# Kernel optimization log

Hardware: AMD Instinct MI355X
Metric: run time of the kernel (lower is better)

## Reference

```python
import jax, jax.numpy as jnp
import numpy as np
from jax import lax

B, DIN, DOUT, DEPTH = 4096, 2048, 2048, 16


def setup_inputs() -> dict:
    key = jax.random.key(0)
    k1, k2, k3, k4 = jax.random.split(key, 4)
    return {
        "x": jax.random.normal(k1, (B, DIN), jnp.float32),
        "absolute_weights": jax.random.normal(k2, (DEPTH, DIN, DOUT), jnp.float32),
        "classical_weights": jax.random.normal(k3, (DIN, DOUT), jnp.float32),
        "classical_biases": jax.random.normal(k4, (DOUT,), jnp.float32),
    }


def _absolute_probs(W):
    # W: [depth, din, dout]; the torch code indexes W[d, j, g] with j over
    # output dims and g in {0,1,2} (3 gates per depth step).
    din = W.shape[1]
    dout = DOUT
    # angles per output j, flattened over (depth, gate): [dout, depth*3]
    ang = jnp.transpose(W[:, :dout, :3], (1, 0, 2)).reshape(dout, -1)
    s0 = jnp.ones((din,), W.dtype) / np.float32(np.sqrt(din))

    def step(s, a):
        # The dense "rotation" matrix built in torch is: diag=cos,
        # superdiag (wrapped) = -sin, subdiag (wrapped) = +sin, i.e.
        # (M s)[i] = cos*s[i] - sin*s[(i+1)%n] + sin*s[(i-1)%n].
        c, si = jnp.cos(a), jnp.sin(a)
        s_new = c * s - si * jnp.roll(s, -1) + si * jnp.roll(s, 1)
        return s_new, None

    def per_j(angs):
        s, _ = lax.scan(step, s0, angs)
        return jnp.abs(s[0]) ** 2

    return jax.vmap(per_j)(ang)  # [dout]


def reference(x, absolute_weights, classical_weights, classical_biases):
    classical = x @ classical_weights + classical_biases  # [B, dout]
    probs = _absolute_probs(absolute_weights)             # [dout], batch-independent
    return jnp.tanh(classical + probs[None, :])
```

## Files before the change

kernel.cpp:

```cpp
#include <hip/hip_runtime.h>
#include <math.h>

#define BATCH 4096
#define DIN   2048
#define DOUT  2048
#define DEPTH 16

typedef unsigned short u16;
typedef __attribute__((ext_vector_type(8))) short short8;
typedef __attribute__((ext_vector_type(16))) float f32x16;


__device__ static inline unsigned bf16_rn(float x) {
    unsigned u = __float_as_uint(x);
    return (u + 0x7FFFu + ((u >> 16) & 1u)) >> 16;
}

__device__ static inline float tanh_fast(float z) {
    float zc = fminf(fmaxf(z, -15.0f), 15.0f);
    float e = __builtin_amdgcn_exp2f(zc * 2.8853900817779268f);
    return (e - 1.0f) * __builtin_amdgcn_rcpf(e + 1.0f);
}

__device__ static inline void async16(u16* lds, const u16* g) {
    __builtin_amdgcn_global_load_lds(
        (const __attribute__((address_space(1))) void*)g,
        (__attribute__((address_space(3))) void*)lds, 16, 0, 0);
}

__global__ __launch_bounds__(256) void probs_kernel(const float* __restrict__ W,
                                                    float* __restrict__ probs) {
    int tid = threadIdx.x;
    int jl = tid >> 4, d = tid & 15;
    int j = blockIdx.x * 16 + jl;
    const float* p = W + (size_t)d * DIN * DOUT + (size_t)j * DOUT;
    float pr = cosf(p[0]) * cosf(p[1]) * cosf(p[2]);
#pragma unroll
    for (int off = 1; off < 16; off <<= 1) pr *= __shfl_xor(pr, off, 16);
    if (d == 0) probs[j] = pr * pr * (1.0f / (float)DIN);
}

__global__ __launch_bounds__(256) void convert_x_kernel(const float* __restrict__ x,
                                                        u16* __restrict__ xh,
                                                        u16* __restrict__ xl) {
    int i = (blockIdx.x * 256 + threadIdx.x) * 4;
    float4 v = *(const float4*)(x + i);
    float vv[4] = {v.x, v.y, v.z, v.w};
    u16 hh[4], ll[4];
#pragma unroll
    for (int c = 0; c < 4; ++c) {
        unsigned hb = bf16_rn(vv[c]);
        hh[c] = (u16)hb;
        float r = vv[c] - __uint_as_float(hb << 16);
        ll[c] = (u16)bf16_rn(r);
    }
    ushort4 h, l;
    h.x = hh[0]; h.y = hh[1]; h.z = hh[2]; h.w = hh[3];
    l.x = ll[0]; l.y = ll[1]; l.z = ll[2]; l.w = ll[3];
    *(ushort4*)(xh + i) = h;
    *(ushort4*)(xl + i) = l;
}

__global__ __launch_bounds__(256) void transpose_w_kernel(const float* __restrict__ W,
                                                          u16* __restrict__ wh,
                                                          u16* __restrict__ wl) {
    __shared__ float t[32][33];
    int n0 = blockIdx.x * 32, k0 = blockIdx.y * 32;
    int tx = threadIdx.x & 31, ty = threadIdx.x >> 5;
#pragma unroll
    for (int i = 0; i < 4; ++i)
        t[ty + i * 8][tx] = W[(size_t)(k0 + ty + i * 8) * DOUT + n0 + tx];
    __syncthreads();
#pragma unroll
    for (int i = 0; i < 4; ++i) {
        float v = t[tx][ty + i * 8];
        size_t o = (size_t)(n0 + ty + i * 8) * DIN + k0 + tx;
        unsigned hb = bf16_rn(v);
        wh[o] = (u16)hb;
        float r = v - __uint_as_float(hb << 16);
        wl[o] = (u16)bf16_rn(r);
    }
}

__global__ __launch_bounds__(256, 2) void gemm_mfma_kernel(
    const u16* __restrict__ xh, const u16* __restrict__ xl,
    const u16* __restrict__ wh, const u16* __restrict__ wl,
    const float* __restrict__ bias, const float* __restrict__ probs,
    float* __restrict__ C)
{
    __shared__ u16 sAh[4096];
    __shared__ u16 sAl[4096];
    __shared__ u16 sBh[4096];
    __shared__ u16 sBl[4096];

    const int tid = threadIdx.x;
    const int lane = tid & 63;
    const int wave = tid >> 6;
    const int bR = blockIdx.y * 128;
    const int bC = blockIdx.x * 128;

    const u16* gsrc = (wave == 0) ? xh + (size_t)bR * DIN
                    : (wave == 1) ? xl + (size_t)bR * DIN
                    : (wave == 2) ? wh + (size_t)bC * DIN
                                  : wl + (size_t)bC * DIN;
    u16* lbase = (wave == 0) ? sAh : (wave == 1) ? sAl : (wave == 2) ? sBh : sBl;

    int goff[8];
#pragma unroll
    for (int i = 0; i < 8; ++i) {
        int row = i * 16 + (lane >> 2);
        int lq = (lane & 3) ^ ((row >> 1) & 3);
        goff[i] = row * DIN + lq * 8;
    }

    const int wm = wave >> 1, wn = wave & 1;
    const int colL = lane & 31;
    const int half = lane >> 5;

    int aoff[2][2], boff[2][2];
#pragma unroll
    for (int mt = 0; mt < 2; ++mt)
#pragma unroll
        for (int c = 0; c < 2; ++c) {
            int r = wm * 64 + mt * 32 + colL;
            int q = (c * 2 + half) ^ ((r >> 1) & 3);
            aoff[mt][c] = r * 32 + q * 8;
        }
#pragma unroll
    for (int nt = 0; nt < 2; ++nt)
#pragma unroll
        for (int c = 0; c < 2; ++c) {
            int r = wn * 64 + nt * 32 + colL;
            int q = (c * 2 + half) ^ ((r >> 1) & 3);
            boff[nt][c] = r * 32 + q * 8;
        }

    f32x16 acc[2][2];
#pragma unroll
    for (int mt = 0; mt < 2; ++mt)
#pragma unroll
        for (int nt = 0; nt < 2; ++nt)
#pragma unroll
            for (int r = 0; r < 16; ++r) acc[mt][nt][r] = 0.f;

    for (int k0 = 0; k0 < DIN; k0 += 32) {
        __syncthreads();
#pragma unroll
        for (int i = 0; i < 8; ++i)
            async16(lbase + i * 512, gsrc + goff[i] + k0);
        __syncthreads();

        short8 ah[2][2], al[2][2], bh[2][2], bl[2][2];
#pragma unroll
        for (int mt = 0; mt < 2; ++mt)
#pragma unroll
            for (int c = 0; c < 2; ++c) {
                ah[mt][c] = *(const short8*)&sAh[aoff[mt][c]];
                al[mt][c] = *(const short8*)&sAl[aoff[mt][c]];
            }
#pragma unroll
        for (int nt = 0; nt < 2; ++nt)
#pragma unroll
            for (int c = 0; c < 2; ++c) {
                bh[nt][c] = *(const short8*)&sBh[boff[nt][c]];
                bl[nt][c] = *(const short8*)&sBl[boff[nt][c]];
            }

#pragma unroll
        for (int mt = 0; mt < 2; ++mt)
#pragma unroll
            for (int nt = 0; nt < 2; ++nt)
#pragma unroll
                for (int c = 0; c < 2; ++c) {
                    acc[mt][nt] = __builtin_amdgcn_mfma_f32_32x32x16_bf16(
                        ah[mt][c], bh[nt][c], acc[mt][nt], 0, 0, 0);
                    acc[mt][nt] = __builtin_amdgcn_mfma_f32_32x32x16_bf16(
                        ah[mt][c], bl[nt][c], acc[mt][nt], 0, 0, 0);
                    acc[mt][nt] = __builtin_amdgcn_mfma_f32_32x32x16_bf16(
                        al[mt][c], bh[nt][c], acc[mt][nt], 0, 0, 0);
                }
    }

#pragma unroll
    for (int nt = 0; nt < 2; ++nt) {
        int ccol = bC + wn * 64 + nt * 32 + colL;
        float bp = bias[ccol] + probs[ccol];
#pragma unroll
        for (int mt = 0; mt < 2; ++mt) {
#pragma unroll
            for (int reg = 0; reg < 16; ++reg) {
                int rrow = bR + wm * 64 + mt * 32 + 4 * half + (reg & 3) + 8 * (reg >> 2);
                C[(size_t)rrow * DOUT + ccol] = tanh_fast(acc[mt][nt][reg] + bp);
            }
        }
    }
}

extern "C" void kernel_launch(void* const* d_in, const int* in_sizes, int n_in,
                              void* d_out, int out_size, void* d_ws, size_t ws_size,
                              hipStream_t stream) {
    const float* x  = (const float*)d_in[0];
    const float* W  = (const float*)d_in[1];
    const float* cw = (const float*)d_in[2];
    const float* cb = (const float*)d_in[3];
    float* out = (float*)d_out;

    const size_t PROBS_B = 8192;
    const size_t XSZ = (size_t)BATCH * DIN;
    const size_t WSZ = (size_t)DIN * DOUT;

    float* probs = (float*)d_ws;
    u16* xh = (u16*)((char*)d_ws + PROBS_B);
    u16* xl = xh + XSZ;
    u16* wh = xl + XSZ;
    u16* wl = wh + WSZ;

    probs_kernel<<<DOUT / 16, 256, 0, stream>>>(W, probs);
    convert_x_kernel<<<XSZ / 4 / 256, 256, 0, stream>>>(x, xh, xl);
    transpose_w_kernel<<<dim3(DOUT / 32, DIN / 32), 256, 0, stream>>>(cw, wh, wl);

    dim3 grid(DOUT / 128, BATCH / 128);
    gemm_mfma_kernel<<<grid, 256, 0, stream>>>(xh, xl, wh, wl, cb, probs, out);
}
```

Baseline: 447.1 us.

## Shrink GEMM tile to 128x64 with 16x16x32 MFMA and fold bias into probs

The GEMM tile is halved in N (128x64), giving twice as many blocks, and the 32x32x16 MFMA is swapped for 16x16x32 with 4x2 subtiles per wave. Launch bounds are raised to 4 blocks per CU to improve occupancy and latency hiding. The bias is now added to probs in the probs kernel, so the epilogue reads one vector instead of two. The cost is lower operand reuse per block, more global/LDS traffic per FLOP, and the smaller MFMA shape may be less efficient.

```diff
diff --git a/kernel.cpp b/kernel.cpp
--- a/kernel.cpp
+++ b/kernel.cpp
@@ -8,7 +8,7 @@
 
 typedef unsigned short u16;
 typedef __attribute__((ext_vector_type(8))) short short8;
-typedef __attribute__((ext_vector_type(16))) float f32x16;
+typedef __attribute__((ext_vector_type(4))) float f32x4;
 
 
 __device__ static inline unsigned bf16_rn(float x) {
@@ -29,7 +29,8 @@
 }
 
 __global__ __launch_bounds__(256) void probs_kernel(const float* __restrict__ W,
-                                                    float* __restrict__ probs) {
+                                                    const float* __restrict__ cb,
+                                                    float* __restrict__ bp) {
     int tid = threadIdx.x;
     int jl = tid >> 4, d = tid & 15;
     int j = blockIdx.x * 16 + jl;
@@ -37,7 +38,7 @@
     float pr = cosf(p[0]) * cosf(p[1]) * cosf(p[2]);
 #pragma unroll
     for (int off = 1; off < 16; off <<= 1) pr *= __shfl_xor(pr, off, 16);
-    if (d == 0) probs[j] = pr * pr * (1.0f / (float)DIN);
+    if (d == 0) bp[j] = pr * pr * (1.0f / (float)DIN) + cb[j];
 }
 
 __global__ __launch_bounds__(256) void convert_x_kernel(const float* __restrict__ x,
@@ -82,28 +83,28 @@
     }
 }
 
-__global__ __launch_bounds__(256, 2) void gemm_mfma_kernel(
+__global__ __launch_bounds__(256, 4) void gemm_mfma_kernel(
     const u16* __restrict__ xh, const u16* __restrict__ xl,
     const u16* __restrict__ wh, const u16* __restrict__ wl,
-    const float* __restrict__ bias, const float* __restrict__ probs,
-    float* __restrict__ C)
+    const float* __restrict__ bp, float* __restrict__ C)
 {
     __shared__ u16 sAh[4096];
     __shared__ u16 sAl[4096];
-    __shared__ u16 sBh[4096];
-    __shared__ u16 sBl[4096];
+    __shared__ u16 sBh[2048];
+    __shared__ u16 sBl[2048];
 
     const int tid = threadIdx.x;
     const int lane = tid & 63;
     const int wave = tid >> 6;
     const int bR = blockIdx.y * 128;
-    const int bC = blockIdx.x * 128;
+    const int bC = blockIdx.x * 64;
 
     const u16* gsrc = (wave == 0) ? xh + (size_t)bR * DIN
                     : (wave == 1) ? xl + (size_t)bR * DIN
                     : (wave == 2) ? wh + (size_t)bC * DIN
                                   : wl + (size_t)bC * DIN;
     u16* lbase = (wave == 0) ? sAh : (wave == 1) ? sAl : (wave == 2) ? sBh : sBl;
+    const int nchunk = (wave < 2) ? 8 : 4;
 
     int goff[8];
 #pragma unroll
@@ -114,86 +115,73 @@
     }
 
     const int wm = wave >> 1, wn = wave & 1;
-    const int colL = lane & 31;
-    const int half = lane >> 5;
-
-    int aoff[2][2], boff[2][2];
-#pragma unroll
-    for (int mt = 0; mt < 2; ++mt)
-#pragma unroll
-        for (int c = 0; c < 2; ++c) {
-            int r = wm * 64 + mt * 32 + colL;
-            int q = (c * 2 + half) ^ ((r >> 1) & 3);
-            aoff[mt][c] = r * 32 + q * 8;
-        }
-#pragma unroll
-    for (int nt = 0; nt < 2; ++nt)
-#pragma unroll
-        for (int c = 0; c < 2; ++c) {
-            int r = wn * 64 + nt * 32 + colL;
-            int q = (c * 2 + half) ^ ((r >> 1) & 3);
-            boff[nt][c] = r * 32 + q * 8;
-        }
-
-    f32x16 acc[2][2];
-#pragma unroll
-    for (int mt = 0; mt < 2; ++mt)
-#pragma unroll
-        for (int nt = 0; nt < 2; ++nt)
-#pragma unroll
-            for (int r = 0; r < 16; ++r) acc[mt][nt][r] = 0.f;
+    const int colL = lane & 15, quad = lane >> 4;
+
+    int aoff[4], boff[2];
+#pragma unroll
+    for (int mt = 0; mt < 4; ++mt) {
+        int r = wm * 64 + mt * 16 + colL;
+        aoff[mt] = r * 32 + (quad ^ ((r >> 1) & 3)) * 8;
+    }
+#pragma unroll
+    for (int nt = 0; nt < 2; ++nt) {
+        int r = wn * 32 + nt * 16 + colL;
+        boff[nt] = r * 32 + (quad ^ ((r >> 1) & 3)) * 8;
+    }
+
+    f32x4 acc[4][2];
+#pragma unroll
+    for (int mt = 0; mt < 4; ++mt)
+#pragma unroll
+        for (int nt = 0; nt < 2; ++nt) acc[mt][nt] = (f32x4){0.f, 0.f, 0.f, 0.f};
 
     for (int k0 = 0; k0 < DIN; k0 += 32) {
         __syncthreads();
 #pragma unroll
         for (int i = 0; i < 8; ++i)
-            async16(lbase + i * 512, gsrc + goff[i] + k0);
+            if (i < nchunk) async16(lbase + i * 512, gsrc + goff[i] + k0);
         __syncthreads();
 
-        short8 ah[2][2], al[2][2], bh[2][2], bl[2][2];
-#pragma unroll
-        for (int mt = 0; mt < 2; ++mt)
-#pragma unroll
-            for (int c = 0; c < 2; ++c) {
-                ah[mt][c] = *(const short8*)&sAh[aoff[mt][c]];
-                al[mt][c] = *(const short8*)&sAl[aoff[mt][c]];
+        short8 ah[4], al[4], bh[2], bl[2];
+#pragma unroll
+        for (int mt = 0; mt < 4; ++mt) {
+            ah[mt] = *(const short8*)&sAh[aoff[mt]];
+            al[mt] = *(const short8*)&sAl[aoff[mt]];
+        }
+#pragma unroll
+        for (int nt = 0; nt < 2; ++nt) {
+            bh[nt] = *(const short8*)&sBh[boff[nt]];
+            bl[nt] = *(const short8*)&sBl[boff[nt]];
+        }
+
+#pragma unroll
+        for (int mt = 0; mt < 4; ++mt)
+#pragma unroll
+            for (int nt = 0; nt < 2; ++nt) {
+                acc[mt][nt] = __builtin_amdgcn_mfma_f32_16x16x32_bf16(
+                    ah[mt], bh[nt], acc[mt][nt], 0, 0, 0);
+                acc[mt][nt] = __builtin_amdgcn_mfma_f32_16x16x32_bf16(
+                    ah[mt], bl[nt], acc[mt][nt], 0, 0, 0);
+                acc[mt][nt] = __builtin_amdgcn_mfma_f32_16x16x32_bf16(
+                    al[mt], bh[nt], acc[mt][nt], 0, 0, 0);
             }
-#pragma unroll
-        for (int nt = 0; nt < 2; ++nt)
-#pragma unroll
-            for (int c = 0; c < 2; ++c) {
-                bh[nt][c] = *(const short8*)&sBh[boff[nt][c]];
-                bl[nt][c] = *(const short8*)&sBl[boff[nt][c]];
-            }
-
-#pragma unroll
-        for (int mt = 0; mt < 2; ++mt)
-#pragma unroll
-            for (int nt = 0; nt < 2; ++nt)
-#pragma unroll
-                for (int c = 0; c < 2; ++c) {
-                    acc[mt][nt] = __builtin_amdgcn_mfma_f32_32x32x16_bf16(
-                        ah[mt][c], bh[nt][c], acc[mt][nt], 0, 0, 0);
-                    acc[mt][nt] = __builtin_amdgcn_mfma_f32_32x32x16_bf16(
-                        ah[mt][c], bl[nt][c], acc[mt][nt], 0, 0, 0);
-                    acc[mt][nt] = __builtin_amdgcn_mfma_f32_32x32x16_bf16(
-                        al[mt][c], bh[nt][c], acc[mt][nt], 0, 0, 0);
-                }
-    }
-
-#pragma unroll
-    for (int nt = 0; nt < 2; ++nt) {
-        int ccol = bC + wn * 64 + nt * 32 + colL;
-        float bp = bias[ccol] + probs[ccol];
-#pragma unroll
-        for (int mt = 0; mt < 2; ++mt) {
-#pragma unroll
-            for (int reg = 0; reg < 16; ++reg) {
-                int rrow = bR + wm * 64 + mt * 32 + 4 * half + (reg & 3) + 8 * (reg >> 2);
-                C[(size_t)rrow * DOUT + ccol] = tanh_fast(acc[mt][nt][reg] + bp);
+    }
+
+    float bpv[2];
+#pragma unroll
+    for (int nt = 0; nt < 2; ++nt)
+        bpv[nt] = bp[bC + wn * 32 + nt * 16 + colL];
+#pragma unroll
+    for (int mt = 0; mt < 4; ++mt)
+#pragma unroll
+        for (int nt = 0; nt < 2; ++nt) {
+            int c = bC + wn * 32 + nt * 16 + colL;
+#pragma unroll
+            for (int reg = 0; reg < 4; ++reg) {
+                int r = bR + wm * 64 + mt * 16 + quad * 4 + reg;
+                C[(size_t)r * DOUT + c] = tanh_fast(acc[mt][nt][reg] + bpv[nt]);
             }
         }
-    }
 }
 
 extern "C" void kernel_launch(void* const* d_in, const int* in_sizes, int n_in,
@@ -209,16 +197,16 @@
     const size_t XSZ = (size_t)BATCH * DIN;
     const size_t WSZ = (size_t)DIN * DOUT;
 
-    float* probs = (float*)d_ws;
+    float* bp = (float*)d_ws;
     u16* xh = (u16*)((char*)d_ws + PROBS_B);
     u16* xl = xh + XSZ;
     u16* wh = xl + XSZ;
     u16* wl = wh + WSZ;
 
-    probs_kernel<<<DOUT / 16, 256, 0, stream>>>(W, probs);
+    probs_kernel<<<DOUT / 16, 256, 0, stream>>>(W, cb, bp);
     convert_x_kernel<<<XSZ / 4 / 256, 256, 0, stream>>>(x, xh, xl);
     transpose_w_kernel<<<dim3(DOUT / 32, DIN / 32), 256, 0, stream>>>(cw, wh, wl);
 
-    dim3 grid(DOUT / 128, BATCH / 128);
-    gemm_mfma_kernel<<<grid, 256, 0, stream>>>(xh, xl, wh, wl, cb, probs, out);
-}
+    dim3 grid(DOUT / 64, BATCH / 128);
+    gemm_mfma_kernel<<<grid, 256, 0, stream>>>(xh, xl, wh, wl, bp, out);
+}
```

Result: slower. 466.0 us (+4.2%).
